# Performance work log

Measured on AMD Instinct MI355X. Metric: run time of the kernel, lower is better.

The kernel has to match this reference:

```python
import jax, jax.numpy as jnp
import numpy as np

B, T, I, H, C = 4096, 64, 60, 60, 600


def setup_inputs() -> dict:
    key = jax.random.key(0)
    ks = jax.random.split(key, 7)
    s = 1.0 / np.sqrt(H).astype(np.float32)  # PyTorch RNN init bound
    u = lambda k, shape: jax.random.uniform(k, shape, jnp.float32, -s, s)
    return {
        "x": jax.random.normal(ks[0], (B, T, I), jnp.float32),
        "w_ih": u(ks[1], (2, 3 * H, I)),   # per-direction [3H, I], gates (r,z,n)
        "w_hh": u(ks[2], (2, 3 * H, H)),
        "b_ih": u(ks[3], (2, 3 * H)),
        "b_hh": u(ks[4], (2, 3 * H)),
        "fc_w": u(ks[5], (C, 2 * H * T)),
        "fc_b": u(ks[6], (C,)),
    }


def _gru_dir(x_tbi, w_ih, w_hh, b_ih, b_hh):
    # Precompute input-side gate pre-activations for all timesteps: [T, B, 3H]
    gx = jnp.einsum('tbi,gi->tbg', x_tbi, w_ih) + b_ih
    h0 = jnp.zeros((x_tbi.shape[1], H), x_tbi.dtype)

    def step(h, gx_t):
        gh = h @ w_hh.T + b_hh                      # [B, 3H]
        r = jax.nn.sigmoid(gx_t[:, :H] + gh[:, :H])
        z = jax.nn.sigmoid(gx_t[:, H:2 * H] + gh[:, H:2 * H])
        n = jnp.tanh(gx_t[:, 2 * H:] + r * gh[:, 2 * H:])
        h_new = (1.0 - z) * n + z * h
        return h_new, h_new

    _, hs = jax.lax.scan(step, h0, gx)
    return hs  # [T, B, H]


def reference(x, w_ih, w_hh, b_ih, b_hh, fc_w, fc_b):
    xt = jnp.swapaxes(x, 0, 1)                        # [T, B, I]
    fwd = _gru_dir(xt, w_ih[0], w_hh[0], b_ih[0], b_hh[0])           # [T,B,H]
    bwd = _gru_dir(xt[::-1], w_ih[1], w_hh[1], b_ih[1], b_hh[1])[::-1]
    out = jnp.concatenate([fwd, bwd], axis=-1)        # [T, B, 2H]
    out = jnp.swapaxes(out, 0, 1).reshape(x.shape[0], -1)  # [B, T*2H]
    return out @ fc_w.T + fc_b
```

## Files before the change

kernel.cpp:

```cpp
#include <hip/hip_runtime.h>

#define BB 4096
#define TT 64
#define NH 60
#define KF 7680
#define NC 600

typedef short bf16x8 __attribute__((ext_vector_type(8)));
typedef float f32x4 __attribute__((ext_vector_type(4)));
#define MFMA16(A,B,C) __builtin_amdgcn_mfma_f32_16x16x32_bf16(A,B,C,0,0,0)

__device__ __forceinline__ unsigned short f2bf(float v) {
    unsigned int u = __float_as_uint(v);
    return (unsigned short)((u + 0x7FFFu + ((u >> 16) & 1u)) >> 16);
}
__device__ __forceinline__ float bf2f(unsigned short b) {
    return __uint_as_float(((unsigned int)b) << 16);
}
__device__ __forceinline__ float sigf(float v)     { return 1.f / (1.f + __expf(-v)); }
__device__ __forceinline__ float tanhfast(float v) { return 2.f / (1.f + __expf(-2.f * v)) - 1.f; }

__global__ __launch_bounds__(512, 2) void gru3_kernel(
    const float* __restrict__ x,
    const float* __restrict__ w_ih,
    const float* __restrict__ w_hh,
    const float* __restrict__ b_ih,
    const float* __restrict__ b_hh,
    unsigned int* __restrict__ hs)
{
    __shared__ unsigned short XHh[32 * 128];
    __shared__ unsigned short XHl[32 * 128];
    __shared__ unsigned int hstage[32][60];

    const int tid = threadIdx.x;
    const int d  = blockIdx.y;
    const int b0 = blockIdx.x * 32;
    const int wave = tid >> 6, lane = tid & 63;
    const int mtile = wave >> 2, ug = wave & 3;
    const int l15 = lane & 15, lq = lane >> 4;
    const int j = ug * 16 + l15;
    const bool jv = j < NH;
    const int m = mtile * 16 + l15;
    const int rbase = mtile * 16 + lq * 4;

    for (int i = tid; i < 32 * 128; i += 512) { XHh[i] = 0; XHl[i] = 0; }

    bf16x8 wHf[3][4], wLf[3][4];
#pragma unroll
    for (int g = 0; g < 3; ++g) {
#pragma unroll
        for (int kt = 0; kt < 4; ++kt) {
            bf16x8 h8, l8;
            const int kb = kt * 32 + lq * 8;
#pragma unroll
            for (int e = 0; e < 8; ++e) {
                const int k = kb + e;
                float v = 0.f;
                if (jv) {
                    if (k < 60)                    v = w_ih[(size_t)d * 10800 + (g * 60 + j) * 60 + k];
                    else if (k >= 64 && k < 124)   v = w_hh[(size_t)d * 10800 + (g * 60 + j) * 60 + (k - 64)];
                }
                const unsigned short hb = f2bf(v);
                const unsigned short lb = f2bf(v - bf2f(hb));
                h8[e] = (short)hb; l8[e] = (short)lb;
            }
            wHf[g][kt] = h8; wLf[g][kt] = l8;
        }
    }

    float bir = 0, biz = 0, bin = 0, bhr = 0, bhz = 0, bhn = 0;
    if (jv) {
        bir = b_ih[d * 180 + j]; biz = b_ih[d * 180 + 60 + j]; bin = b_ih[d * 180 + 120 + j];
        bhr = b_hh[d * 180 + j]; bhz = b_hh[d * 180 + 60 + j]; bhn = b_hh[d * 180 + 120 + j];
    }

    const bool xact = tid < 480;
    const int rowx = xact ? tid / 15 : 31;
    const int cx   = xact ? tid % 15 : 14;
    const float* xb = x + ((size_t)(b0 + rowx) * TT) * 60 + cx * 4;
    unsigned int* hsb = hs + (size_t)(b0 + rowx) * KF + d * 60 + cx * 4;

    __syncthreads();

    if (xact) {
        const int tt0 = d ? (TT - 1) : 0;
        const float4 v = *(const float4*)(xb + tt0 * 60);
        const float vv[4] = {v.x, v.y, v.z, v.w};
#pragma unroll
        for (int e = 0; e < 4; ++e) {
            const int k = cx * 4 + e;
            const int idx = rowx * 128 + (((k >> 3) ^ (rowx & 7)) << 3) + (k & 7);
            const unsigned short hb = f2bf(vv[e]);
            XHh[idx] = hb; XHl[idx] = f2bf(vv[e] - bf2f(hb));
        }
    }
    float hold[4] = {0.f, 0.f, 0.f, 0.f};
    __syncthreads();

    for (int s = 0; s < TT; ++s) {
        const int tt = d ? (TT - 1 - s) : s;
        float4 xp = make_float4(0.f, 0.f, 0.f, 0.f);
        const bool morex = (s < TT - 1) && xact;
        if (morex) xp = *(const float4*)(xb + (d ? (TT - 2 - s) : (s + 1)) * 60);

        f32x4 aR = {0,0,0,0}, aZ = {0,0,0,0}, aNX = {0,0,0,0}, aNH = {0,0,0,0};
#pragma unroll
        for (int kt = 0; kt < 4; ++kt) {
            const int c = kt * 4 + lq;
            const int off = m * 128 + ((c ^ (m & 7)) << 3);
            const bf16x8 aH = *(const bf16x8*)(XHh + off);
            const bf16x8 aL = *(const bf16x8*)(XHl + off);
            aR = MFMA16(aH, wHf[0][kt], aR); aR = MFMA16(aH, wLf[0][kt], aR); aR = MFMA16(aL, wHf[0][kt], aR);
            aZ = MFMA16(aH, wHf[1][kt], aZ); aZ = MFMA16(aH, wLf[1][kt], aZ); aZ = MFMA16(aL, wHf[1][kt], aZ);
            if (kt < 2) {
                aNX = MFMA16(aH, wHf[2][kt], aNX); aNX = MFMA16(aH, wLf[2][kt], aNX); aNX = MFMA16(aL, wHf[2][kt], aNX);
            } else {
                aNH = MFMA16(aH, wHf[2][kt], aNH); aNH = MFMA16(aH, wLf[2][kt], aNH); aNH = MFMA16(aL, wHf[2][kt], aNH);
            }
        }

        float hnew[4];
#pragma unroll
        for (int r = 0; r < 4; ++r) {
            const float rr = sigf(aR[r] + bir + bhr);
            const float zz = sigf(aZ[r] + biz + bhz);
            const float nn = tanhfast(aNX[r] + bin + rr * (aNH[r] + bhn));
            hnew[r] = (1.f - zz) * nn + zz * hold[r];
            hold[r] = hnew[r];
        }
        __syncthreads();

        if (jv) {
#pragma unroll
            for (int r = 0; r < 4; ++r) {
                const int rw = rbase + r;
                const int k = 64 + j;
                const int idx = rw * 128 + (((k >> 3) ^ (rw & 7)) << 3) + (k & 7);
                const unsigned short hb = f2bf(hnew[r]);
                const unsigned short lb = f2bf(hnew[r] - bf2f(hb));
                XHh[idx] = hb; XHl[idx] = lb;
                hstage[rw][j] = ((unsigned int)hb << 16) | lb;
            }
        }
        if (morex) {
            const float vv[4] = {xp.x, xp.y, xp.z, xp.w};
#pragma unroll
            for (int e = 0; e < 4; ++e) {
                const int k = cx * 4 + e;
                const int idx = rowx * 128 + (((k >> 3) ^ (rowx & 7)) << 3) + (k & 7);
                const unsigned short hb = f2bf(vv[e]);
                XHh[idx] = hb; XHl[idx] = f2bf(vv[e] - bf2f(hb));
            }
        }
        __syncthreads();

        if (xact) {
            const uint4 hv = *(const uint4*)&hstage[rowx][cx * 4];
            *(uint4*)(hsb + (size_t)tt * 120) = hv;
        }
    }
}

__global__ void out_init_kernel(const float* __restrict__ fcb, float* __restrict__ out) {
    const int i = blockIdx.x * 1024 + threadIdx.x;
    out[i] = fcb[i % NC];
}

__global__ __launch_bounds__(512, 2) void fc3_kernel(
    const unsigned int* __restrict__ hs,
    const float* __restrict__ fcw,
    float* __restrict__ out)
{
    __shared__ unsigned short AH[256 * 64], AL[256 * 64];
    __shared__ unsigned short BH[128 * 64], BL[128 * 64];

    const int tid = threadIdx.x;
    const int m0 = blockIdx.x * 256;
    const int n0 = blockIdx.y * 128;
    const int k0 = blockIdx.z * 2560;
    const int wave = tid >> 6, lane = tid & 63;
    const int wm = wave >> 1, wn = wave & 1;
    const int l15 = lane & 15, lq = lane >> 4;

    f32x4 acc[4][4];
#pragma unroll
    for (int a = 0; a < 4; ++a)
#pragma unroll
        for (int b = 0; b < 4; ++b) acc[a][b] = (f32x4){0, 0, 0, 0};

    uint4 pa[8]; float4 pb[4];
#pragma unroll
    for (int it = 0; it < 8; ++it) {
        const int u = tid + it * 512, row = u >> 4, q = u & 15;
        pa[it] = *(const uint4*)(hs + (size_t)(m0 + row) * KF + k0 + q * 4);
    }
#pragma unroll
    for (int it = 0; it < 4; ++it) {
        const int u = tid + it * 512, row = u >> 4, q = u & 15;
        const int cc = n0 + row;
        pb[it] = (cc < NC) ? *(const float4*)(fcw + (size_t)cc * KF + k0 + q * 4)
                           : make_float4(0.f, 0.f, 0.f, 0.f);
    }

    for (int ks = 0; ks < 40; ++ks) {
#pragma unroll
        for (int it = 0; it < 8; ++it) {
            const int u = tid + it * 512, row = u >> 4, q = u & 15;
            const int off = row * 64 + (((q >> 1) ^ (row & 7)) << 3) + (q & 1) * 4;
            const unsigned int av[4] = {pa[it].x, pa[it].y, pa[it].z, pa[it].w};
            uint2 wh, wl;
            wh.x = (av[0] >> 16) | (av[1] & 0xFFFF0000u);
            wh.y = (av[2] >> 16) | (av[3] & 0xFFFF0000u);
            wl.x = (av[0] & 0xFFFFu) | (av[1] << 16);
            wl.y = (av[2] & 0xFFFFu) | (av[3] << 16);
            *(uint2*)(AH + off) = wh;
            *(uint2*)(AL + off) = wl;
        }
#pragma unroll
        for (int it = 0; it < 4; ++it) {
            const int u = tid + it * 512, row = u >> 4, q = u & 15;
            const int off = row * 64 + (((q >> 1) ^ (row & 7)) << 3) + (q & 1) * 4;
            const float bv[4] = {pb[it].x, pb[it].y, pb[it].z, pb[it].w};
            unsigned short h4[4], l4[4];
#pragma unroll
            for (int e = 0; e < 4; ++e) {
                h4[e] = f2bf(bv[e]);
                l4[e] = f2bf(bv[e] - bf2f(h4[e]));
            }
            uint2 wh, wl;
            wh.x = (unsigned int)h4[0] | ((unsigned int)h4[1] << 16);
            wh.y = (unsigned int)h4[2] | ((unsigned int)h4[3] << 16);
            wl.x = (unsigned int)l4[0] | ((unsigned int)l4[1] << 16);
            wl.y = (unsigned int)l4[2] | ((unsigned int)l4[3] << 16);
            *(uint2*)(BH + off) = wh;
            *(uint2*)(BL + off) = wl;
        }
        __syncthreads();

        if (ks + 1 < 40) {
            const int kk = k0 + (ks + 1) * 64;
#pragma unroll
            for (int it = 0; it < 8; ++it) {
                const int u = tid + it * 512, row = u >> 4, q = u & 15;
                pa[it] = *(const uint4*)(hs + (size_t)(m0 + row) * KF + kk + q * 4);
            }
#pragma unroll
            for (int it = 0; it < 4; ++it) {
                const int u = tid + it * 512, row = u >> 4, q = u & 15;
                const int cc = n0 + row;
                pb[it] = (cc < NC) ? *(const float4*)(fcw + (size_t)cc * KF + kk + q * 4)
                                   : make_float4(0.f, 0.f, 0.f, 0.f);
            }
        }

#pragma unroll
        for (int kt = 0; kt < 2; ++kt) {
            bf16x8 aH[4], aL[4], bH[4], bL[4];
            const int ca = kt * 4 + lq;
#pragma unroll
            for (int t = 0; t < 4; ++t) {
                const int mr = wm * 64 + t * 16 + l15;
                const int offa = mr * 64 + ((ca ^ (mr & 7)) << 3);
                aH[t] = *(const bf16x8*)(AH + offa);
                aL[t] = *(const bf16x8*)(AL + offa);
                const int nr = wn * 64 + t * 16 + l15;
                const int offb = nr * 64 + ((ca ^ (nr & 7)) << 3);
                bH[t] = *(const bf16x8*)(BH + offb);
                bL[t] = *(const bf16x8*)(BL + offb);
            }
#pragma unroll
            for (int mt = 0; mt < 4; ++mt)
#pragma unroll
                for (int nt = 0; nt < 4; ++nt) {
                    acc[mt][nt] = MFMA16(aH[mt], bH[nt], acc[mt][nt]);
                    acc[mt][nt] = MFMA16(aH[mt], bL[nt], acc[mt][nt]);
                    acc[mt][nt] = MFMA16(aL[mt], bH[nt], acc[mt][nt]);
                }
        }
        __syncthreads();
    }

#pragma unroll
    for (int mt = 0; mt < 4; ++mt) {
        const int row = m0 + wm * 64 + mt * 16 + lq * 4;
#pragma unroll
        for (int nt = 0; nt < 4; ++nt) {
            const int col = n0 + wn * 64 + nt * 16 + l15;
            if (col < NC) {
#pragma unroll
                for (int r = 0; r < 4; ++r)
                    atomicAdd(out + (size_t)(row + r) * NC + col, acc[mt][nt][r]);
            }
        }
    }
}

extern "C" void kernel_launch(void* const* d_in, const int* in_sizes, int n_in,
                              void* d_out, int out_size, void* d_ws, size_t ws_size,
                              hipStream_t stream) {
    (void)in_sizes; (void)n_in; (void)out_size;
    const float* x    = (const float*)d_in[0];
    const float* w_ih = (const float*)d_in[1];
    const float* w_hh = (const float*)d_in[2];
    const float* b_ih = (const float*)d_in[3];
    const float* b_hh = (const float*)d_in[4];
    const float* fcw  = (const float*)d_in[5];
    const float* fcb  = (const float*)d_in[6];
    float* out = (float*)d_out;
    unsigned int* hs = (unsigned int*)d_ws;

    if (ws_size < (size_t)KF * BB * sizeof(unsigned int)) return;

    out_init_kernel<<<dim3((BB * NC) / 1024), 1024, 0, stream>>>(fcb, out);
    gru3_kernel<<<dim3(BB / 32, 2), 512, 0, stream>>>(x, w_ih, w_hh, b_ih, b_hh, hs);
    fc3_kernel<<<dim3(BB / 256, 5, 3), 512, 0, stream>>>(hs, fcw, out);
}
```

Before: 379.7 us.

## Double-buffer LDS in GRU recurrence and FC GEMM to drop barriers

The GRU kernel now ping-pongs its shared X/H and staging buffers, which removes one __syncthreads per timestep. It also splits the r/z accumulators into two independent chains to shorten MFMA dependencies. The FC kernel switches to double-buffered LDS with 32-wide K stages and packs hi/lo halves into a single 64-wide row. It uses a raw lgkmcnt wait plus s_barrier so global loads and LDS writes overlap with MFMA work. The trade-off is twice the LDS footprint and hand-placed barriers that could cause races if the ordering is wrong.

New measurement: 365.6 us. -3.7%, faster.

```diff
diff --git a/kernel.cpp b/kernel.cpp
--- a/kernel.cpp
+++ b/kernel.cpp
@@ -20,7 +20,7 @@
 __device__ __forceinline__ float sigf(float v)     { return 1.f / (1.f + __expf(-v)); }
 __device__ __forceinline__ float tanhfast(float v) { return 2.f / (1.f + __expf(-2.f * v)) - 1.f; }
 
-__global__ __launch_bounds__(512, 2) void gru3_kernel(
+__global__ __launch_bounds__(512, 2) void gru4_kernel(
     const float* __restrict__ x,
     const float* __restrict__ w_ih,
     const float* __restrict__ w_hh,
@@ -28,9 +28,9 @@
     const float* __restrict__ b_hh,
     unsigned int* __restrict__ hs)
 {
-    __shared__ unsigned short XHh[32 * 128];
-    __shared__ unsigned short XHl[32 * 128];
-    __shared__ unsigned int hstage[32][60];
+    __shared__ unsigned short XHh[2][32 * 128];
+    __shared__ unsigned short XHl[2][32 * 128];
+    __shared__ unsigned int hstage[2][32][60];
 
     const int tid = threadIdx.x;
     const int d  = blockIdx.y;
@@ -43,7 +43,7 @@
     const int m = mtile * 16 + l15;
     const int rbase = mtile * 16 + lq * 4;
 
-    for (int i = tid; i < 32 * 128; i += 512) { XHh[i] = 0; XHl[i] = 0; }
+    for (int i = tid; i < 2 * 32 * 128; i += 512) { (&XHh[0][0])[i] = 0; (&XHl[0][0])[i] = 0; }
 
     bf16x8 wHf[3][4], wLf[3][4];
 #pragma unroll
@@ -91,44 +91,51 @@
             const int k = cx * 4 + e;
             const int idx = rowx * 128 + (((k >> 3) ^ (rowx & 7)) << 3) + (k & 7);
             const unsigned short hb = f2bf(vv[e]);
-            XHh[idx] = hb; XHl[idx] = f2bf(vv[e] - bf2f(hb));
+            XHh[0][idx] = hb; XHl[0][idx] = f2bf(vv[e] - bf2f(hb));
         }
     }
     float hold[4] = {0.f, 0.f, 0.f, 0.f};
     __syncthreads();
 
+#pragma unroll 2
     for (int s = 0; s < TT; ++s) {
+        const int p = s & 1, pn = p ^ 1;
         const int tt = d ? (TT - 1 - s) : s;
+
         float4 xp = make_float4(0.f, 0.f, 0.f, 0.f);
         const bool morex = (s < TT - 1) && xact;
         if (morex) xp = *(const float4*)(xb + (d ? (TT - 2 - s) : (s + 1)) * 60);
 
-        f32x4 aR = {0,0,0,0}, aZ = {0,0,0,0}, aNX = {0,0,0,0}, aNH = {0,0,0,0};
+        f32x4 aR0 = {0,0,0,0}, aR1 = {0,0,0,0}, aZ0 = {0,0,0,0}, aZ1 = {0,0,0,0},
+              aNX = {0,0,0,0}, aNH_ = {0,0,0,0};
+        const unsigned short* Xh = &XHh[p][0];
+        const unsigned short* Xl = &XHl[p][0];
 #pragma unroll
         for (int kt = 0; kt < 4; ++kt) {
             const int c = kt * 4 + lq;
             const int off = m * 128 + ((c ^ (m & 7)) << 3);
-            const bf16x8 aH = *(const bf16x8*)(XHh + off);
-            const bf16x8 aL = *(const bf16x8*)(XHl + off);
-            aR = MFMA16(aH, wHf[0][kt], aR); aR = MFMA16(aH, wLf[0][kt], aR); aR = MFMA16(aL, wHf[0][kt], aR);
-            aZ = MFMA16(aH, wHf[1][kt], aZ); aZ = MFMA16(aH, wLf[1][kt], aZ); aZ = MFMA16(aL, wHf[1][kt], aZ);
+            const bf16x8 aH = *(const bf16x8*)(Xh + off);
+            const bf16x8 aL = *(const bf16x8*)(Xl + off);
             if (kt < 2) {
+                aR0 = MFMA16(aH, wHf[0][kt], aR0); aR0 = MFMA16(aH, wLf[0][kt], aR0); aR0 = MFMA16(aL, wHf[0][kt], aR0);
+                aZ0 = MFMA16(aH, wHf[1][kt], aZ0); aZ0 = MFMA16(aH, wLf[1][kt], aZ0); aZ0 = MFMA16(aL, wHf[1][kt], aZ0);
                 aNX = MFMA16(aH, wHf[2][kt], aNX); aNX = MFMA16(aH, wLf[2][kt], aNX); aNX = MFMA16(aL, wHf[2][kt], aNX);
             } else {
-                aNH = MFMA16(aH, wHf[2][kt], aNH); aNH = MFMA16(aH, wLf[2][kt], aNH); aNH = MFMA16(aL, wHf[2][kt], aNH);
+                aR1 = MFMA16(aH, wHf[0][kt], aR1); aR1 = MFMA16(aH, wLf[0][kt], aR1); aR1 = MFMA16(aL, wHf[0][kt], aR1);
+                aZ1 = MFMA16(aH, wHf[1][kt], aZ1); aZ1 = MFMA16(aH, wLf[1][kt], aZ1); aZ1 = MFMA16(aL, wHf[1][kt], aZ1);
+                aNH_ = MFMA16(aH, wHf[2][kt], aNH_); aNH_ = MFMA16(aH, wLf[2][kt], aNH_); aNH_ = MFMA16(aL, wHf[2][kt], aNH_);
             }
         }
 
         float hnew[4];
 #pragma unroll
         for (int r = 0; r < 4; ++r) {
-            const float rr = sigf(aR[r] + bir + bhr);
-            const float zz = sigf(aZ[r] + biz + bhz);
-            const float nn = tanhfast(aNX[r] + bin + rr * (aNH[r] + bhn));
+            const float rr = sigf(aR0[r] + aR1[r] + bir + bhr);
+            const float zz = sigf(aZ0[r] + aZ1[r] + biz + bhz);
+            const float nn = tanhfast(aNX[r] + bin + rr * (aNH_[r] + bhn));
             hnew[r] = (1.f - zz) * nn + zz * hold[r];
             hold[r] = hnew[r];
         }
-        __syncthreads();
 
         if (jv) {
 #pragma unroll
@@ -138,8 +145,8 @@
                 const int idx = rw * 128 + (((k >> 3) ^ (rw & 7)) << 3) + (k & 7);
                 const unsigned short hb = f2bf(hnew[r]);
                 const unsigned short lb = f2bf(hnew[r] - bf2f(hb));
-                XHh[idx] = hb; XHl[idx] = lb;
-                hstage[rw][j] = ((unsigned int)hb << 16) | lb;
+                XHh[pn][idx] = hb; XHl[pn][idx] = lb;
+                hstage[pn][rw][j] = ((unsigned int)hb << 16) | lb;
             }
         }
         if (morex) {
@@ -149,13 +156,13 @@
                 const int k = cx * 4 + e;
                 const int idx = rowx * 128 + (((k >> 3) ^ (rowx & 7)) << 3) + (k & 7);
                 const unsigned short hb = f2bf(vv[e]);
-                XHh[idx] = hb; XHl[idx] = f2bf(vv[e] - bf2f(hb));
+                XHh[pn][idx] = hb; XHl[pn][idx] = f2bf(vv[e] - bf2f(hb));
             }
         }
         __syncthreads();
 
         if (xact) {
-            const uint4 hv = *(const uint4*)&hstage[rowx][cx * 4];
+            const uint4 hv = *(const uint4*)&hstage[pn][rowx][cx * 4];
             *(uint4*)(hsb + (size_t)tt * 120) = hv;
         }
     }
@@ -166,13 +173,13 @@
     out[i] = fcb[i % NC];
 }
 
-__global__ __launch_bounds__(512, 2) void fc3_kernel(
+__global__ __launch_bounds__(512, 2) void fc4_kernel(
     const unsigned int* __restrict__ hs,
     const float* __restrict__ fcw,
     float* __restrict__ out)
 {
-    __shared__ unsigned short AH[256 * 64], AL[256 * 64];
-    __shared__ unsigned short BH[128 * 64], BL[128 * 64];
+    __shared__ unsigned short Ash[2][256 * 64];
+    __shared__ unsigned short Bsh[2][128 * 64];
 
     const int tid = threadIdx.x;
     const int m0 = blockIdx.x * 256;
@@ -188,96 +195,103 @@
 #pragma unroll
         for (int b = 0; b < 4; ++b) acc[a][b] = (f32x4){0, 0, 0, 0};
 
-    uint4 pa[8]; float4 pb[4];
-#pragma unroll
-    for (int it = 0; it < 8; ++it) {
-        const int u = tid + it * 512, row = u >> 4, q = u & 15;
-        pa[it] = *(const uint4*)(hs + (size_t)(m0 + row) * KF + k0 + q * 4);
-    }
-#pragma unroll
-    for (int it = 0; it < 4; ++it) {
-        const int u = tid + it * 512, row = u >> 4, q = u & 15;
-        const int cc = n0 + row;
-        pb[it] = (cc < NC) ? *(const float4*)(fcw + (size_t)cc * KF + k0 + q * 4)
-                           : make_float4(0.f, 0.f, 0.f, 0.f);
-    }
-
-    for (int ks = 0; ks < 40; ++ks) {
-#pragma unroll
-        for (int it = 0; it < 8; ++it) {
-            const int u = tid + it * 512, row = u >> 4, q = u & 15;
-            const int off = row * 64 + (((q >> 1) ^ (row & 7)) << 3) + (q & 1) * 4;
-            const unsigned int av[4] = {pa[it].x, pa[it].y, pa[it].z, pa[it].w};
-            uint2 wh, wl;
-            wh.x = (av[0] >> 16) | (av[1] & 0xFFFF0000u);
-            wh.y = (av[2] >> 16) | (av[3] & 0xFFFF0000u);
-            wl.x = (av[0] & 0xFFFFu) | (av[1] << 16);
-            wl.y = (av[2] & 0xFFFFu) | (av[3] << 16);
-            *(uint2*)(AH + off) = wh;
-            *(uint2*)(AL + off) = wl;
-        }
-#pragma unroll
-        for (int it = 0; it < 4; ++it) {
-            const int u = tid + it * 512, row = u >> 4, q = u & 15;
-            const int off = row * 64 + (((q >> 1) ^ (row & 7)) << 3) + (q & 1) * 4;
-            const float bv[4] = {pb[it].x, pb[it].y, pb[it].z, pb[it].w};
-            unsigned short h4[4], l4[4];
-#pragma unroll
-            for (int e = 0; e < 4; ++e) {
-                h4[e] = f2bf(bv[e]);
-                l4[e] = f2bf(bv[e] - bf2f(h4[e]));
-            }
-            uint2 wh, wl;
-            wh.x = (unsigned int)h4[0] | ((unsigned int)h4[1] << 16);
-            wh.y = (unsigned int)h4[2] | ((unsigned int)h4[3] << 16);
-            wl.x = (unsigned int)l4[0] | ((unsigned int)l4[1] << 16);
-            wl.y = (unsigned int)l4[2] | ((unsigned int)l4[3] << 16);
-            *(uint2*)(BH + off) = wh;
-            *(uint2*)(BL + off) = wl;
-        }
-        __syncthreads();
-
-        if (ks + 1 < 40) {
-            const int kk = k0 + (ks + 1) * 64;
-#pragma unroll
-            for (int it = 0; it < 8; ++it) {
-                const int u = tid + it * 512, row = u >> 4, q = u & 15;
-                pa[it] = *(const uint4*)(hs + (size_t)(m0 + row) * KF + kk + q * 4);
-            }
-#pragma unroll
-            for (int it = 0; it < 4; ++it) {
-                const int u = tid + it * 512, row = u >> 4, q = u & 15;
-                const int cc = n0 + row;
-                pb[it] = (cc < NC) ? *(const float4*)(fcw + (size_t)cc * KF + kk + q * 4)
-                                   : make_float4(0.f, 0.f, 0.f, 0.f);
-            }
-        }
-
-#pragma unroll
-        for (int kt = 0; kt < 2; ++kt) {
-            bf16x8 aH[4], aL[4], bH[4], bL[4];
-            const int ca = kt * 4 + lq;
-#pragma unroll
-            for (int t = 0; t < 4; ++t) {
-                const int mr = wm * 64 + t * 16 + l15;
-                const int offa = mr * 64 + ((ca ^ (mr & 7)) << 3);
-                aH[t] = *(const bf16x8*)(AH + offa);
-                aL[t] = *(const bf16x8*)(AL + offa);
-                const int nr = wn * 64 + t * 16 + l15;
-                const int offb = nr * 64 + ((ca ^ (nr & 7)) << 3);
-                bH[t] = *(const bf16x8*)(BH + offb);
-                bL[t] = *(const bf16x8*)(BL + offb);
-            }
-#pragma unroll
-            for (int mt = 0; mt < 4; ++mt)
-#pragma unroll
-                for (int nt = 0; nt < 4; ++nt) {
-                    acc[mt][nt] = MFMA16(aH[mt], bH[nt], acc[mt][nt]);
-                    acc[mt][nt] = MFMA16(aH[mt], bL[nt], acc[mt][nt]);
-                    acc[mt][nt] = MFMA16(aL[mt], bH[nt], acc[mt][nt]);
-                }
-        }
-        __syncthreads();
+    uint4 pa[4]; float4 pb[2];
+
+#define STAGE_LOAD(t) do {                                                          \
+    const int kc_ = k0 + (t) * 32;                                                  \
+    _Pragma("unroll")                                                               \
+    for (int it = 0; it < 4; ++it) {                                                \
+        const int g_ = tid + it * 512, row_ = g_ >> 3, qi_ = g_ & 7;                \
+        pa[it] = *(const uint4*)(hs + (size_t)(m0 + row_) * KF + kc_ + qi_ * 4);    \
+    }                                                                               \
+    _Pragma("unroll")                                                               \
+    for (int it = 0; it < 2; ++it) {                                                \
+        const int g_ = tid + it * 512, row_ = g_ >> 3, qi_ = g_ & 7;                \
+        const int cc_ = n0 + row_;                                                  \
+        pb[it] = (cc_ < NC) ? *(const float4*)(fcw + (size_t)cc_ * KF + kc_ + qi_ * 4) \
+                            : make_float4(0.f, 0.f, 0.f, 0.f);                      \
+    }                                                                               \
+} while (0)
+
+#define STAGE_WRITE(buf) do {                                                       \
+    _Pragma("unroll")                                                               \
+    for (int it = 0; it < 4; ++it) {                                                \
+        const int g_ = tid + it * 512, row_ = g_ >> 3, qi_ = g_ & 7;                \
+        const int ch_ = qi_ >> 1, hf_ = qi_ & 1;                                    \
+        unsigned short* base_ = &Ash[buf][row_ * 64];                               \
+        uint2 wh_, wl_;                                                             \
+        wh_.x = (pa[it].x >> 16) | (pa[it].y & 0xFFFF0000u);                        \
+        wh_.y = (pa[it].z >> 16) | (pa[it].w & 0xFFFF0000u);                        \
+        wl_.x = (pa[it].x & 0xFFFFu) | (pa[it].y << 16);                            \
+        wl_.y = (pa[it].z & 0xFFFFu) | (pa[it].w << 16);                            \
+        *(uint2*)(base_ + ((ch_ ^ (row_ & 7)) << 3) + hf_ * 4) = wh_;               \
+        *(uint2*)(base_ + (((ch_ | 4) ^ (row_ & 7)) << 3) + hf_ * 4) = wl_;         \
+    }                                                                               \
+    _Pragma("unroll")                                                               \
+    for (int it = 0; it < 2; ++it) {                                                \
+        const int g_ = tid + it * 512, row_ = g_ >> 3, qi_ = g_ & 7;                \
+        const int ch_ = qi_ >> 1, hf_ = qi_ & 1;                                    \
+        unsigned short* base_ = &Bsh[buf][row_ * 64];                               \
+        const float bv_[4] = {pb[it].x, pb[it].y, pb[it].z, pb[it].w};              \
+        unsigned short h4_[4], l4_[4];                                              \
+        _Pragma("unroll")                                                           \
+        for (int e = 0; e < 4; ++e) { h4_[e] = f2bf(bv_[e]); l4_[e] = f2bf(bv_[e] - bf2f(h4_[e])); } \
+        uint2 wh_, wl_;                                                             \
+        wh_.x = (unsigned int)h4_[0] | ((unsigned int)h4_[1] << 16);                \
+        wh_.y = (unsigned int)h4_[2] | ((unsigned int)h4_[3] << 16);                \
+        wl_.x = (unsigned int)l4_[0] | ((unsigned int)l4_[1] << 16);                \
+        wl_.y = (unsigned int)l4_[2] | ((unsigned int)l4_[3] << 16);                \
+        *(uint2*)(base_ + ((ch_ ^ (row_ & 7)) << 3) + hf_ * 4) = wh_;               \
+        *(uint2*)(base_ + (((ch_ | 4) ^ (row_ & 7)) << 3) + hf_ * 4) = wl_;         \
+    }                                                                               \
+} while (0)
+
+#define MFMA_PHASE(buf) do {                                                        \
+    const unsigned short* Ab_ = &Ash[buf][0];                                       \
+    const unsigned short* Bb_ = &Bsh[buf][0];                                       \
+    bf16x8 aH_[4], aL_[4], bH_[4], bL_[4];                                          \
+    _Pragma("unroll")                                                               \
+    for (int t = 0; t < 4; ++t) {                                                   \
+        const int mr_ = wm * 64 + t * 16 + l15;                                     \
+        const unsigned short* p_ = Ab_ + mr_ * 64;                                  \
+        aH_[t] = *(const bf16x8*)(p_ + ((lq ^ (mr_ & 7)) << 3));                    \
+        aL_[t] = *(const bf16x8*)(p_ + (((lq | 4) ^ (mr_ & 7)) << 3));              \
+        const int nr_ = wn * 64 + t * 16 + l15;                                     \
+        const unsigned short* q_ = Bb_ + nr_ * 64;                                  \
+        bH_[t] = *(const bf16x8*)(q_ + ((lq ^ (nr_ & 7)) << 3));                    \
+        bL_[t] = *(const bf16x8*)(q_ + (((lq | 4) ^ (nr_ & 7)) << 3));              \
+    }                                                                               \
+    _Pragma("unroll")                                                               \
+    for (int mt = 0; mt < 4; ++mt)                                                  \
+        _Pragma("unroll")                                                           \
+        for (int nt = 0; nt < 4; ++nt) {                                            \
+            acc[mt][nt] = MFMA16(aH_[mt], bH_[nt], acc[mt][nt]);                    \
+            acc[mt][nt] = MFMA16(aH_[mt], bL_[nt], acc[mt][nt]);                    \
+            acc[mt][nt] = MFMA16(aL_[mt], bH_[nt], acc[mt][nt]);                    \
+        }                                                                           \
+} while (0)
+
+#define BARRIER_LGKM() do {                                                         \
+    asm volatile("s_waitcnt lgkmcnt(0)" ::: "memory");                              \
+    __builtin_amdgcn_s_barrier();                                                   \
+    __builtin_amdgcn_sched_barrier(0);                                              \
+} while (0)
+
+    STAGE_LOAD(0);
+    STAGE_WRITE(0);
+    STAGE_LOAD(1);
+    __syncthreads();
+
+#pragma unroll 1
+    for (int t = 0; t < 80; t += 2) {
+        STAGE_WRITE(1);
+        if (t + 2 < 80) STAGE_LOAD(t + 2);
+        MFMA_PHASE(0);
+        BARRIER_LGKM();
+        if (t + 2 < 80) STAGE_WRITE(0);
+        if (t + 3 < 80) STAGE_LOAD(t + 3);
+        MFMA_PHASE(1);
+        BARRIER_LGKM();
     }
 
 #pragma unroll
@@ -293,6 +307,10 @@
             }
         }
     }
+#undef STAGE_LOAD
+#undef STAGE_WRITE
+#undef MFMA_PHASE
+#undef BARRIER_LGKM
 }
 
 extern "C" void kernel_launch(void* const* d_in, const int* in_sizes, int n_in,
@@ -312,6 +330,6 @@
     if (ws_size < (size_t)KF * BB * sizeof(unsigned int)) return;
 
     out_init_kernel<<<dim3((BB * NC) / 1024), 1024, 0, stream>>>(fcb, out);
-    gru3_kernel<<<dim3(BB / 32, 2), 512, 0, stream>>>(x, w_ih, w_hh, b_ih, b_hh, hs);
-    fc3_kernel<<<dim3(BB / 256, 5, 3), 512, 0, stream>>>(hs, fcw, out);
-}
+    gru4_kernel<<<dim3(BB / 32, 2), 512, 0, stream>>>(x, w_ih, w_hh, b_ih, b_hh, hs);
+    fc4_kernel<<<dim3(BB / 256, 5, 3), 512, 0, stream>>>(hs, fcw, out);
+}
```
